# Optimization experiments

Hardware: AMD Instinct MI355X
Metric: run time of the kernel (lower is better)

The kernel has to match this reference:

```python
import jax, jax.numpy as jnp
import numpy as np

N = 100000   # nodes per node type (A and B)
E = 500000   # edges per relation
H = 8        # n_heads
D = 32       # hidden_dim (= encoder_hidden_dim = input_dim)
IN = 32      # input feature dim
SLOPE = 0.2  # leaky relu negative slope
# relations in order: ab1 (A->B), ba1 (B->A), ab2 (A->B), ba2 (B->A)
RELS = [(0, 1), (1, 0), (0, 1), (1, 0)]  # (src_type, dst_type)
REV = [1, 0, 3, 2]                        # reverse-relation index


def _leaky(x):
    return jnp.where(x >= 0, x, SLOPE * x)


def _rel_conv(h_src, h_dst, W_src, W_dst, remb, Wr, s_idx, d_idx):
    """RelationGraphConv: GAT-style edge attention on one relation graph."""
    fs = (h_src @ W_src).reshape(-1, H, D)          # [N, H, D]
    fd = (h_dst @ W_dst).reshape(-1, H, D)          # [N, H, D]
    ra = (remb @ Wr).reshape(H, 2 * D)              # [H, 2D]
    e_dst = (fd * ra[:, :D]).sum(-1)                # [N, H]
    e_src = (fs * ra[:, D:]).sum(-1)                # [N, H]
    e = _leaky(e_src[s_idx] + e_dst[d_idx])         # [E, H]
    # edge softmax per destination node (per head)
    m = jax.ops.segment_max(e, d_idx, num_segments=N)
    m = jnp.where(jnp.isfinite(m), m, 0.0)
    ex = jnp.exp(e - m[d_idx])
    z = jax.ops.segment_sum(ex, d_idx, num_segments=N)
    a = ex / z[d_idx]                               # [E, H]
    msg = fs[s_idx] * a[:, :, None]                 # [E, H, D]
    out = jax.ops.segment_sum(msg, d_idx, num_segments=N)  # [N, H, D]
    return jax.nn.relu(out.reshape(N, H * D))


def _crossing(stacked, w):
    """RelationCrossing over relations targeting one dst type.
    stacked: [R, N, H*D], w: [H, D]"""
    f = stacked.reshape(stacked.shape[0], N, H, D)
    att = (f * w).sum(-1, keepdims=True)            # [R, N, H, 1]
    att = jax.nn.softmax(_leaky(att), axis=0)
    return (f * att).sum(0).reshape(N, H * D)


def setup_inputs() -> dict:
    key = jax.random.key(0)
    ks = jax.random.split(key, 12)
    xn = lambda k, shape, s=1.0: jax.random.normal(k, shape, jnp.float32) * s
    return {
        "feat":    xn(ks[0], (4, N, IN)),
        "rel_emb": xn(ks[1], (4, IN)),
        "W_node":  xn(ks[2], (2, IN, H * D), 0.1),
        "W_rel":   xn(ks[3], (4, IN, H * 2 * D), 0.1),
        "W_prop":  xn(ks[4], (4, IN, H * D), 0.1),
        "b_prop":  xn(ks[5], (4, H * D), 0.1),
        "W_res":   xn(ks[6], (2, IN, H * D), 0.1),
        "b_res":   xn(ks[7], (2, H * D), 0.1),
        "alpha":   xn(ks[8], (2,)),
        "Wx":      xn(ks[9], (2, H, D), 0.1),
        "src": jax.random.randint(ks[10], (4, E), 0, N),
        "dst": jax.random.randint(ks[11], (4, E), 0, N),
    }


def reference(feat, rel_emb, W_node, W_rel, W_prop, b_prop, W_res, b_res,
              alpha, Wx, src, dst):
    outs = []
    for r in range(4):  # fixed small set of relations
        st, dt = RELS[r]
        # src feats come from the reverse relation's dst-node features
        o = _rel_conv(feat[REV[r]], feat[r], W_node[st], W_node[dt],
                      rel_emb[r], W_rel[r], src[r], dst[r])
        # residual connection (eval mode, dropout = identity)
        a = jax.nn.sigmoid(alpha[dt])
        res = feat[r] @ W_res[dt] + b_res[dt]
        outs.append(o * a + res * (1.0 - a))
    # relation crossing per dst node type
    cross_A = _crossing(jnp.stack([outs[1], outs[3]]), Wx[0])
    cross_B = _crossing(jnp.stack([outs[0], outs[2]]), Wx[1])
    node_out = jnp.stack([cross_A, cross_B])                  # [2, N, H*D]
    # relation propagation (Linear per etype)
    rel_out = jnp.einsum('ri,rio->ro', rel_emb, W_prop) + b_prop  # [4, H*D]
    return node_out, rel_out
```

## Files before the change

kernel.cpp:

```cpp
#include <hip/hip_runtime.h>
#include <hip/hip_bf16.h>

#define NN 100000
#define EE 500000
#define H 8
#define D 32
#define INF_ 32
#define HD 256
#define SLOPE 0.2f
#define L_ (4 * NN)
#define NB_ ((L_ + 255) / 256)

typedef unsigned short u16;
typedef unsigned int u32;
typedef short bf16x8 __attribute__((ext_vector_type(8)));
typedef float f32x4 __attribute__((ext_vector_type(4)));

union U8 { uint4 u; bf16x8 v; };

__device__ __forceinline__ float leaky(float x) { return x >= 0.f ? x : SLOPE * x; }
__device__ __forceinline__ u16 bf16r(float x) {
    u32 u = __float_as_uint(x);
    u += 0x7fffu + ((u >> 16) & 1u);
    return (u16)(u >> 16);
}
__device__ __forceinline__ float bf16f(u16 v) { return __uint_as_float((u32)v << 16); }
__device__ __forceinline__ u32 cvtpk(float lo, float hi) {
    u32 r;
    asm("v_cvt_pk_bf16_f32 %0, %1, %2" : "=v"(r) : "v"(lo), "v"(hi));
    return r;
}

__global__ void k_prep(const float* __restrict__ rel_emb, const float* __restrict__ W_rel,
                       const float* __restrict__ W_prop, const float* __restrict__ b_prop,
                       float* __restrict__ ra, float* __restrict__ rel_out) {
    int idx = blockIdx.x * blockDim.x + threadIdx.x;
    if (idx < 4 * 512) {
        int r = idx >> 9, o = idx & 511;
        float s = 0.f;
        #pragma unroll
        for (int i = 0; i < INF_; ++i) s += rel_emb[r * INF_ + i] * W_rel[(r * INF_ + i) * 512 + o];
        ra[idx] = s;
    } else if (idx < 4 * 512 + 4 * 256) {
        int j = idx - 2048;
        int r = j >> 8;
        float s = b_prop[j];
        #pragma unroll
        for (int i = 0; i < INF_; ++i) s += rel_emb[r * INF_ + i] * W_prop[(r * INF_ + i) * 256 + (j & 255)];
        rel_out[j] = s;
    }
}

__global__ void k_wfrag(const float* __restrict__ W_node, const float* __restrict__ W_res,
                        const float* __restrict__ ra, u16* __restrict__ Wfrag) {
    int idx = blockIdx.x * 256 + threadIdx.x;
    if (idx >= 68 * 512) return;
    int lb = idx & 511;
    int l = lb >> 3, b = lb & 7;
    int k = (l >> 4) * 8 + b, i = l & 15;
    float v;
    if (idx < 4 * 512) {
        int q = idx >> 9;
        int rq = q ^ 1;
        const float* W = W_node + (size_t)(q & 1) * 32 * 256;
        int h = i & 7;
        const float* rr = (i < 8) ? (ra + q * 512 + h * 64 + 32) : (ra + rq * 512 + h * 64);
        float s = 0.f;
        #pragma unroll
        for (int j = 0; j < 32; ++j) s += W[k * 256 + h * 32 + j] * rr[j];
        v = s;
    } else if (idx < 36 * 512) {
        int j = idx - 4 * 512;
        int ty = j >> 13;
        int ct = (j & 8191) >> 9;
        v = W_node[(size_t)ty * 32 * 256 + k * 256 + ct * 16 + i];
    } else {
        int j = idx - 36 * 512;
        int ty = j >> 13;
        int ct = (j & 8191) >> 9;
        v = W_res[(size_t)ty * 32 * 256 + k * 256 + ct * 16 + i];
    }
    Wfrag[idx] = bf16r(v);
}

__global__ __launch_bounds__(256) void k_score(const float* __restrict__ feat,
                                               const u16* __restrict__ Wfrag,
                                               float* __restrict__ e_src,
                                               float* __restrict__ e_dst,
                                               u16* __restrict__ featb) {
    const int q = blockIdx.y, rq = q ^ 1;
    const int t = threadIdx.x, lane = t & 63;
    const int li = lane & 15, g = lane >> 4;
    const int wid = blockIdx.x * 4 + (t >> 6);
    const int nw = gridDim.x * 4;
    f32x4 zz = {0.f, 0.f, 0.f, 0.f};
    U8 a;
    a.u = *(const uint4*)(Wfrag + ((size_t)q * 64 + lane) * 8);
    const float* F = feat + (size_t)rq * NN * INF_;
    u16* Fb = featb + (size_t)rq * NN * INF_;
    for (int tile = wid; tile < NN / 16; tile += nw) {
        const int node = tile * 16 + li;
        const float* fp = F + node * 32 + g * 8;
        float4 f0 = *(const float4*)fp;
        float4 f1 = *(const float4*)(fp + 4);
        U8 b;
        b.u.x = cvtpk(f0.x, f0.y); b.u.y = cvtpk(f0.z, f0.w);
        b.u.z = cvtpk(f1.x, f1.y); b.u.w = cvtpk(f1.z, f1.w);
        *(uint4*)(Fb + node * 32 + g * 8) = b.u;
        f32x4 sc = __builtin_amdgcn_mfma_f32_16x16x32_bf16(a.v, b.v, zz, 0, 0, 0);
        float* sp = (g < 2) ? (e_src + ((size_t)q * NN + node) * 8 + (g & 1) * 4)
                            : (e_dst + ((size_t)rq * NN + node) * 8 + (g & 1) * 4);
        *(float4*)sp = make_float4(sc[0], sc[1], sc[2], sc[3]);
    }
}

__global__ void k_count(const int* __restrict__ dst, u32* __restrict__ deg, u32* __restrict__ epos) {
    int idx = blockIdx.x * blockDim.x + threadIdx.x;
    if (idx >= 4 * EE) return;
    int r = idx / EE;
    epos[idx] = atomicAdd(&deg[r * NN + dst[idx]], 1u);
}

__global__ void k_scan1(const u32* __restrict__ deg, u32* __restrict__ incl, u32* __restrict__ bsum) {
    __shared__ u32 sm[256];
    const int t = threadIdx.x;
    int i = blockIdx.x * 256 + t;
    u32 v = (i < L_) ? deg[i] : 0u;
    sm[t] = v;
    __syncthreads();
    for (int ofs = 1; ofs < 256; ofs <<= 1) {
        u32 x = (t >= ofs) ? sm[t - ofs] : 0u;
        __syncthreads();
        sm[t] += x;
        __syncthreads();
    }
    if (i < L_) incl[i] = sm[t];
    if (t == 255) bsum[blockIdx.x] = sm[255];
}

__global__ void k_scan2(const u32* __restrict__ bsum, u32* __restrict__ bofs) {
    __shared__ u32 sm[256];
    __shared__ u32 runS;
    const int t = threadIdx.x;
    if (t == 0) runS = 0u;
    __syncthreads();
    for (int c = 0; c < NB_; c += 256) {
        u32 v = (c + t < NB_) ? bsum[c + t] : 0u;
        sm[t] = v;
        __syncthreads();
        for (int ofs = 1; ofs < 256; ofs <<= 1) {
            u32 x = (t >= ofs) ? sm[t - ofs] : 0u;
            __syncthreads();
            sm[t] += x;
            __syncthreads();
        }
        u32 excl = sm[t] - v;
        if (c + t < NB_) bofs[c + t] = runS + excl;
        __syncthreads();
        if (t == 255) runS += sm[255];
        __syncthreads();
    }
}

__global__ void k_scan3(const u32* __restrict__ deg, const u32* __restrict__ incl,
                        const u32* __restrict__ bofs, u32* __restrict__ offsets) {
    int i = blockIdx.x * 256 + threadIdx.x;
    if (i >= L_) return;
    offsets[i] = incl[i] - deg[i] + bofs[i >> 8];
}

__global__ void k_fill(const int* __restrict__ src, const int* __restrict__ dst,
                       const u32* __restrict__ offsets, const u32* __restrict__ epos,
                       int* __restrict__ esorted) {
    int idx = blockIdx.x * blockDim.x + threadIdx.x;
    if (idx >= 4 * EE) return;
    int r = idx / EE;
    esorted[offsets[r * NN + dst[idx]] + epos[idx]] = src[idx];
}

template <int W>
__device__ __forceinline__ void procW(const int* __restrict__ ep,
                                      const float* __restrict__ esr,
                                      const u16* __restrict__ Fb,
                                      int h, int fq, float ed,
                                      float& z, float& a0, float& a1, float& a2, float& a3) {
    int s[W];
    #pragma unroll
    for (int j = 0; j < W; ++j) s[j] = ep[j];
    float e[W];
    ushort4 f[W];
    #pragma unroll
    for (int j = 0; j < W; ++j) {
        e[j] = esr[(size_t)s[j] * 8 + h];
        f[j] = *(const ushort4*)(Fb + (size_t)s[j] * INF_ + fq * 4);
    }
    float w[W];
    #pragma unroll
    for (int j = 0; j < W; ++j) w[j] = __expf(leaky(e[j] + ed));
    #pragma unroll
    for (int j = 0; j < W; ++j) {
        z += w[j];
        a0 = fmaf(bf16f(f[j].x), w[j], a0);
        a1 = fmaf(bf16f(f[j].y), w[j], a1);
        a2 = fmaf(bf16f(f[j].z), w[j], a2);
        a3 = fmaf(bf16f(f[j].w), w[j], a3);
    }
}

__global__ __launch_bounds__(256) void k_msg_final(const u32* __restrict__ offsets,
                                                   const u32* __restrict__ deg,
                                                   const int* __restrict__ esorted,
                                                   const float* __restrict__ e_src,
                                                   const float* __restrict__ e_dst,
                                                   const u16* __restrict__ featb,
                                                   const u16* __restrict__ Wfrag,
                                                   const float* __restrict__ b_res,
                                                   const float* __restrict__ alpha,
                                                   const float* __restrict__ Wx,
                                                   float* __restrict__ outp) {
    const int ty = blockIdx.y;
    const int rA = ty ? 0 : 1, rB = ty ? 2 : 3;
    const int t = threadIdx.x, lane = t & 63, w = t >> 6;
    const int tile = blockIdx.x;
    __shared__ uint4 lag[2][16][33];

    {
        const int h = lane >> 3, fq = lane & 7;
        #pragma unroll 1
        for (int uu = 0; uu < 8; ++uu) {
            const int unit = uu * 4 + w;
            const int rs = unit >> 4, nl = unit & 15;
            const int r = rs ? rB : rA;
            const int node = tile * 16 + nl;
            const int i = r * NN + node;
            const u32 off = offsets[i], dg = deg[i];
            uint2 st = {0u, 0u};
            if (dg) {
                const float ed = e_dst[(size_t)i * 8 + h];
                const float* esr = e_src + (size_t)r * NN * 8;
                const u16* Fb = featb + (size_t)(r ^ 1) * NN * INF_;
                const int* ep = esorted + off;
                float z = 0.f, a0 = 0.f, a1 = 0.f, a2 = 0.f, a3 = 0.f;
                u32 k = 0;
                for (; k + 8 <= dg; k += 8)
                    procW<8>(ep + k, esr, Fb, h, fq, ed, z, a0, a1, a2, a3);
                u32 rem = dg - k;
                if (rem & 4) { procW<4>(ep + k, esr, Fb, h, fq, ed, z, a0, a1, a2, a3); k += 4; }
                if (rem & 2) { procW<2>(ep + k, esr, Fb, h, fq, ed, z, a0, a1, a2, a3); k += 2; }
                if (rem & 1) { procW<1>(ep + k, esr, Fb, h, fq, ed, z, a0, a1, a2, a3); }
                float inv = 1.f / z;
                st.x = cvtpk(a0 * inv, a1 * inv);
                st.y = cvtpk(a2 * inv, a3 * inv);
            }
            *((uint2*)lag[rs][nl] + h * 8 + fq) = st;
        }
    }
    __syncthreads();

    const int li = lane & 15, g = lane >> 4;
    const int node = tile * 16 + li;
    const float ga = 1.f / (1.f + __expf(-alpha[ty]));
    const float gb = 1.f - ga;
    f32x4 zz = {0.f, 0.f, 0.f, 0.f};
    const u16* WnF = Wfrag + (size_t)(4 + (1 - ty) * 16) * 512;
    const u16* WrF = Wfrag + (size_t)(36 + ty * 16) * 512;
    const u16* FbA = featb + (size_t)rA * NN * INF_;
    const u16* FbB = featb + (size_t)rB * NN * INF_;

    U8 fA, fB;
    fA.u = *(const uint4*)(FbA + (size_t)node * 32 + g * 8);
    fB.u = *(const uint4*)(FbB + (size_t)node * 32 + g * 8);
    float* op = outp + ((size_t)ty * NN + node) * HD;

    #pragma unroll
    for (int hh = 0; hh < 2; ++hh) {
        const int h = w + hh * 4;
        U8 ag1, ag2;
        ag1.u = lag[0][li][h * 4 + g];
        ag2.u = lag[1][li][h * 4 + g];
        float o1[8], o2[8];
        float s1 = 0.f, s2 = 0.f;
        #pragma unroll
        for (int c2 = 0; c2 < 2; ++c2) {
            const int ct = h * 2 + c2;
            U8 wn, wr;
            wn.u = *(const uint4*)(WnF + ((size_t)ct * 64 + lane) * 8);
            wr.u = *(const uint4*)(WrF + ((size_t)ct * 64 + lane) * 8);
            f32x4 m1 = __builtin_amdgcn_mfma_f32_16x16x32_bf16(wn.v, ag1.v, zz, 0, 0, 0);
            f32x4 m2 = __builtin_amdgcn_mfma_f32_16x16x32_bf16(wn.v, ag2.v, zz, 0, 0, 0);
            f32x4 r1 = __builtin_amdgcn_mfma_f32_16x16x32_bf16(wr.v, fA.v, zz, 0, 0, 0);
            f32x4 r2 = __builtin_amdgcn_mfma_f32_16x16x32_bf16(wr.v, fB.v, zz, 0, 0, 0);
            float4 bv = *(const float4*)(b_res + ty * 256 + ct * 16 + g * 4);
            float4 wv = *(const float4*)(Wx + ty * 256 + ct * 16 + g * 4);
            #pragma unroll
            for (int j = 0; j < 4; ++j) {
                float bj = (&bv.x)[j], wj = (&wv.x)[j];
                float v1 = fmaxf(m1[j], 0.f) * ga + (r1[j] + bj) * gb;
                float v2 = fmaxf(m2[j], 0.f) * ga + (r2[j] + bj) * gb;
                o1[c2 * 4 + j] = v1;
                o2[c2 * 4 + j] = v2;
                s1 += v1 * wj;
                s2 += v2 * wj;
            }
        }
        s1 += __shfl_xor(s1, 16, 64);
        s1 += __shfl_xor(s1, 32, 64);
        s2 += __shfl_xor(s2, 16, 64);
        s2 += __shfl_xor(s2, 32, 64);
        float a1l = leaky(s1), a2l = leaky(s2);
        float mx = fmaxf(a1l, a2l);
        float e1 = __expf(a1l - mx), e2 = __expf(a2l - mx);
        float inv = 1.f / (e1 + e2);
        float wa = e1 * inv, wb = e2 * inv;
        #pragma unroll
        for (int c2 = 0; c2 < 2; ++c2) {
            const int ct = h * 2 + c2;
            float4 o;
            #pragma unroll
            for (int j = 0; j < 4; ++j)
                (&o.x)[j] = o1[c2 * 4 + j] * wa + o2[c2 * 4 + j] * wb;
            *(float4*)(op + ct * 16 + g * 4) = o;
        }
    }
}

extern "C" void kernel_launch(void* const* d_in, const int* in_sizes, int n_in,
                              void* d_out, int out_size, void* d_ws, size_t ws_size,
                              hipStream_t stream) {
    const float* feat    = (const float*)d_in[0];
    const float* rel_emb = (const float*)d_in[1];
    const float* W_node  = (const float*)d_in[2];
    const float* W_rel   = (const float*)d_in[3];
    const float* W_prop  = (const float*)d_in[4];
    const float* b_prop  = (const float*)d_in[5];
    const float* W_res   = (const float*)d_in[6];
    const float* b_res   = (const float*)d_in[7];
    const float* alpha   = (const float*)d_in[8];
    const float* Wx      = (const float*)d_in[9];
    const int*   src     = (const int*)d_in[10];
    const int*   dst     = (const int*)d_in[11];
    float* out = (float*)d_out;

    char* ws = (char*)d_ws;
    float* ra      = (float*)ws;
    float* e_src   = (float*)(ws + 8192);
    float* e_dst   = e_src + (size_t)4 * NN * H;
    u16*   featb   = (u16*)(e_dst + (size_t)4 * NN * H);
    u16*   Wfrag   = featb + (size_t)4 * NN * INF_;
    u32*   deg     = (u32*)(Wfrag + 68 * 512);
    u32*   offsets = deg + L_;
    u32*   incl    = offsets + L_;
    u32*   bsum    = incl + L_;
    u32*   bofs    = bsum + 2048;
    u32*   epos    = bofs + 2048;
    int*   esorted = (int*)(epos + (size_t)4 * EE);

    hipMemsetAsync(deg, 0, (size_t)L_ * 4, stream);

    k_prep<<<12, 256, 0, stream>>>(rel_emb, W_rel, W_prop, b_prop, ra, out + (size_t)2 * NN * HD);
    k_wfrag<<<136, 256, 0, stream>>>(W_node, W_res, ra, Wfrag);

    int eb = (4 * EE + 255) / 256;
    k_count<<<eb, 256, 0, stream>>>(dst, deg, epos);
    k_scan1<<<NB_, 256, 0, stream>>>(deg, incl, bsum);
    k_scan2<<<1, 256, 0, stream>>>(bsum, bofs);
    k_scan3<<<NB_, 256, 0, stream>>>(deg, incl, bofs, offsets);
    k_fill<<<eb, 256, 0, stream>>>(src, dst, offsets, epos, esorted);

    k_score<<<dim3(512, 4), 256, 0, stream>>>(feat, Wfrag, e_src, e_dst, featb);

    k_msg_final<<<dim3(NN / 16, 2), 256, 0, stream>>>(offsets, deg, esorted, e_src, e_dst,
                                                      featb, Wfrag, b_res, alpha, Wx, out);
}
```

Measured before the change: 444.5 us.

## Pack per-node scores and bf16 features into 128-byte records for gathers

Interleaves e_src, the bf16 source features and e_dst for each node into a single 128-byte record, so each edge gather reads one cache line instead of touching two separate arrays. The offsets and degrees for a tile are also loaded once per wave and distributed with shuffles rather than reloaded per unit. This adds padding-free but tightly coupled indexing, since the record for relation q holds features of type q^1 and e_dst of relation q^1.

```diff
diff --git a/kernel.cpp b/kernel.cpp
--- a/kernel.cpp
+++ b/kernel.cpp
@@ -85,9 +85,7 @@
 
 __global__ __launch_bounds__(256) void k_score(const float* __restrict__ feat,
                                                const u16* __restrict__ Wfrag,
-                                               float* __restrict__ e_src,
-                                               float* __restrict__ e_dst,
-                                               u16* __restrict__ featb) {
+                                               char* __restrict__ pk) {
     const int q = blockIdx.y, rq = q ^ 1;
     const int t = threadIdx.x, lane = t & 63;
     const int li = lane & 15, g = lane >> 4;
@@ -97,7 +95,7 @@
     U8 a;
     a.u = *(const uint4*)(Wfrag + ((size_t)q * 64 + lane) * 8);
     const float* F = feat + (size_t)rq * NN * INF_;
-    u16* Fb = featb + (size_t)rq * NN * INF_;
+    char* pkq = pk + (size_t)q * NN * 128;
     for (int tile = wid; tile < NN / 16; tile += nw) {
         const int node = tile * 16 + li;
         const float* fp = F + node * 32 + g * 8;
@@ -106,10 +104,10 @@
         U8 b;
         b.u.x = cvtpk(f0.x, f0.y); b.u.y = cvtpk(f0.z, f0.w);
         b.u.z = cvtpk(f1.x, f1.y); b.u.w = cvtpk(f1.z, f1.w);
-        *(uint4*)(Fb + node * 32 + g * 8) = b.u;
+        char* rec = pkq + (size_t)node * 128;
+        *(uint4*)(rec + 32 + g * 16) = b.u;
         f32x4 sc = __builtin_amdgcn_mfma_f32_16x16x32_bf16(a.v, b.v, zz, 0, 0, 0);
-        float* sp = (g < 2) ? (e_src + ((size_t)q * NN + node) * 8 + (g & 1) * 4)
-                            : (e_dst + ((size_t)rq * NN + node) * 8 + (g & 1) * 4);
+        char* sp = rec + ((g < 2) ? g * 16 : 96 + (g - 2) * 16);
         *(float4*)sp = make_float4(sc[0], sc[1], sc[2], sc[3]);
     }
 }
@@ -180,8 +178,7 @@
 
 template <int W>
 __device__ __forceinline__ void procW(const int* __restrict__ ep,
-                                      const float* __restrict__ esr,
-                                      const u16* __restrict__ Fb,
+                                      const char* __restrict__ pkr,
                                       int h, int fq, float ed,
                                       float& z, float& a0, float& a1, float& a2, float& a3) {
     int s[W];
@@ -191,8 +188,9 @@
     ushort4 f[W];
     #pragma unroll
     for (int j = 0; j < W; ++j) {
-        e[j] = esr[(size_t)s[j] * 8 + h];
-        f[j] = *(const ushort4*)(Fb + (size_t)s[j] * INF_ + fq * 4);
+        const char* rec = pkr + (size_t)s[j] * 128;
+        e[j] = *(const float*)(rec + h * 4);
+        f[j] = *(const ushort4*)(rec + 32 + fq * 8);
     }
     float w[W];
     #pragma unroll
@@ -210,9 +208,7 @@
 __global__ __launch_bounds__(256) void k_msg_final(const u32* __restrict__ offsets,
                                                    const u32* __restrict__ deg,
                                                    const int* __restrict__ esorted,
-                                                   const float* __restrict__ e_src,
-                                                   const float* __restrict__ e_dst,
-                                                   const u16* __restrict__ featb,
+                                                   const char* __restrict__ pk,
                                                    const u16* __restrict__ Wfrag,
                                                    const float* __restrict__ b_res,
                                                    const float* __restrict__ alpha,
@@ -224,6 +220,13 @@
     const int tile = blockIdx.x;
     __shared__ uint4 lag[2][16][33];
 
+    u32 odv;
+    {
+        int seg = lane >> 4, nl0 = lane & 15;
+        int ii = ((seg < 2) ? rA : rB) * NN + tile * 16 + nl0;
+        odv = (seg & 1) ? deg[ii] : offsets[ii];
+    }
+
     {
         const int h = lane >> 3, fq = lane & 7;
         #pragma unroll 1
@@ -232,22 +235,21 @@
             const int rs = unit >> 4, nl = unit & 15;
             const int r = rs ? rB : rA;
             const int node = tile * 16 + nl;
-            const int i = r * NN + node;
-            const u32 off = offsets[i], dg = deg[i];
+            const u32 off = __shfl(odv, (rs << 5) + nl, 64);
+            const u32 dg  = __shfl(odv, (rs << 5) + 16 + nl, 64);
             uint2 st = {0u, 0u};
             if (dg) {
-                const float ed = e_dst[(size_t)i * 8 + h];
-                const float* esr = e_src + (size_t)r * NN * 8;
-                const u16* Fb = featb + (size_t)(r ^ 1) * NN * INF_;
+                const float ed = *(const float*)(pk + ((size_t)(r ^ 1) * NN + node) * 128 + 96 + h * 4);
+                const char* pkr = pk + (size_t)r * NN * 128;
                 const int* ep = esorted + off;
                 float z = 0.f, a0 = 0.f, a1 = 0.f, a2 = 0.f, a3 = 0.f;
                 u32 k = 0;
                 for (; k + 8 <= dg; k += 8)
-                    procW<8>(ep + k, esr, Fb, h, fq, ed, z, a0, a1, a2, a3);
+                    procW<8>(ep + k, pkr, h, fq, ed, z, a0, a1, a2, a3);
                 u32 rem = dg - k;
-                if (rem & 4) { procW<4>(ep + k, esr, Fb, h, fq, ed, z, a0, a1, a2, a3); k += 4; }
-                if (rem & 2) { procW<2>(ep + k, esr, Fb, h, fq, ed, z, a0, a1, a2, a3); k += 2; }
-                if (rem & 1) { procW<1>(ep + k, esr, Fb, h, fq, ed, z, a0, a1, a2, a3); }
+                if (rem & 4) { procW<4>(ep + k, pkr, h, fq, ed, z, a0, a1, a2, a3); k += 4; }
+                if (rem & 2) { procW<2>(ep + k, pkr, h, fq, ed, z, a0, a1, a2, a3); k += 2; }
+                if (rem & 1) { procW<1>(ep + k, pkr, h, fq, ed, z, a0, a1, a2, a3); }
                 float inv = 1.f / z;
                 st.x = cvtpk(a0 * inv, a1 * inv);
                 st.y = cvtpk(a2 * inv, a3 * inv);
@@ -264,12 +266,10 @@
     f32x4 zz = {0.f, 0.f, 0.f, 0.f};
     const u16* WnF = Wfrag + (size_t)(4 + (1 - ty) * 16) * 512;
     const u16* WrF = Wfrag + (size_t)(36 + ty * 16) * 512;
-    const u16* FbA = featb + (size_t)rA * NN * INF_;
-    const u16* FbB = featb + (size_t)rB * NN * INF_;
 
     U8 fA, fB;
-    fA.u = *(const uint4*)(FbA + (size_t)node * 32 + g * 8);
-    fB.u = *(const uint4*)(FbB + (size_t)node * 32 + g * 8);
+    fA.u = *(const uint4*)(pk + ((size_t)(rA ^ 1) * NN + node) * 128 + 32 + g * 16);
+    fB.u = *(const uint4*)(pk + ((size_t)(rB ^ 1) * NN + node) * 128 + 32 + g * 16);
     float* op = outp + ((size_t)ty * NN + node) * HD;
 
     #pragma unroll
@@ -343,11 +343,9 @@
 
     char* ws = (char*)d_ws;
     float* ra      = (float*)ws;
-    float* e_src   = (float*)(ws + 8192);
-    float* e_dst   = e_src + (size_t)4 * NN * H;
-    u16*   featb   = (u16*)(e_dst + (size_t)4 * NN * H);
-    u16*   Wfrag   = featb + (size_t)4 * NN * INF_;
-    u32*   deg     = (u32*)(Wfrag + 68 * 512);
+    char*  pk      = ws + 8192;
+    u16*   Wfrag   = (u16*)(pk + (size_t)4 * NN * 128);
+    u32*   deg     = (u32*)((char*)Wfrag + 68 * 512 * 2);
     u32*   offsets = deg + L_;
     u32*   incl    = offsets + L_;
     u32*   bsum    = incl + L_;
@@ -367,8 +365,8 @@
     k_scan3<<<NB_, 256, 0, stream>>>(deg, incl, bofs, offsets);
     k_fill<<<eb, 256, 0, stream>>>(src, dst, offsets, epos, esorted);
 
-    k_score<<<dim3(512, 4), 256, 0, stream>>>(feat, Wfrag, e_src, e_dst, featb);
-
-    k_msg_final<<<dim3(NN / 16, 2), 256, 0, stream>>>(offsets, deg, esorted, e_src, e_dst,
-                                                      featb, Wfrag, b_res, alpha, Wx, out);
-}
+    k_score<<<dim3(512, 4), 256, 0, stream>>>(feat, Wfrag, pk);
+
+    k_msg_final<<<dim3(NN / 16, 2), 256, 0, stream>>>(offsets, deg, esorted, pk,
+                                                      Wfrag, b_res, alpha, Wx, out);
+}
```

Result: faster. 417.7 us (median of 2 runs) (-6.0%).
